# Kernel optimization log

Measured on AMD Instinct MI355X. Metric: run time of the kernel, lower is better.

Reference implementation:

```python
import jax, jax.numpy as jnp
import numpy as np

B, C, H, W = 1, 96, 512, 512
WS, HEADS, SHIFT = 8, 6, 4  # index=1 -> shift = ws//2


def _rel_pos_index(ws):
    # static numpy computation of Swin relative position index, (N, N) int
    coords = np.stack(np.meshgrid(np.arange(ws), np.arange(ws), indexing='ij'))
    cf = coords.reshape(2, -1)                    # (2, N)
    rel = (cf[:, :, None] - cf[:, None, :]).transpose(1, 2, 0)  # (N, N, 2)
    rel[:, :, 0] += ws - 1
    rel[:, :, 1] += ws - 1
    rel[:, :, 0] *= 2 * ws - 1
    return rel.sum(-1)                            # (N, N)


def _attn_mask(h, w, ws, shift):
    # static numpy replication of calculate_mask (shift>0 assumed meaningful)
    img = np.zeros((h, w), np.float32)
    sl = (slice(0, -ws), slice(-ws, -shift), slice(-shift, None))
    cnt = 0
    for hs in sl:
        for wcol in sl:
            img[hs, wcol] = cnt
            cnt += 1
    mw = img.reshape(h // ws, ws, w // ws, ws).transpose(0, 2, 1, 3).reshape(-1, ws * ws)
    am = mw[:, None, :] - mw[:, :, None]          # (nW, N, N)
    return np.where(am != 0, np.float32(-100.0), np.float32(0.0))


def setup_inputs() -> dict:
    key = jax.random.key(0)
    ks = jax.random.split(key, 5)
    return {
        "x": jax.random.normal(ks[0], (B, C, H, W), jnp.float32),
        "rel_bias_table": jax.random.normal(ks[1], ((2 * WS - 1) ** 2, HEADS), jnp.float32) * 0.02,
        "w_qkv": jax.random.normal(ks[2], (3 * C, C), jnp.float32) * 0.02,
        "b_qkv": jnp.zeros((3 * C,), jnp.float32),
        "w_proj": jax.random.normal(ks[3], (C, C), jnp.float32) * 0.02,
        "b_proj": jnp.zeros((C,), jnp.float32),
        "window_size": WS,
        "num_heads": HEADS,
        "shift_size": SHIFT,
    }


def reference(x, rel_bias_table, w_qkv, b_qkv, w_proj, b_proj, window_size, num_heads, shift_size):
    b, c, h, w = x.shape
    ws = window_size
    n = ws * ws
    hd = c // num_heads
    scale = hd ** -0.5

    # faithful to original: raw reshape (B,C,H,W)->(B,H,W,C), roll, reshape back
    xv = x.reshape(b, h, w, c)
    if shift_size > 0:
        xv = jnp.roll(xv, (-shift_size, -shift_size), axis=(1, 2))
    xv = xv.reshape(b, c, h, w)

    # window_partition -> (B_, N, C)
    win = xv.reshape(b, c, h // ws, ws, w // ws, ws).transpose(0, 2, 4, 3, 5, 1).reshape(-1, n, c)
    b_ = win.shape[0]

    qkv = (win @ w_qkv.T + b_qkv).reshape(b_, n, 3, num_heads, hd).transpose(2, 0, 3, 1, 4)
    q, k, v = qkv[0] * scale, qkv[1], qkv[2]       # (B_, h, N, hd)

    attn = jnp.einsum('bhnd,bhmd->bhnm', q, k)     # (B_, h, N, N)

    idx = _rel_pos_index(ws)
    bias = rel_bias_table[idx.reshape(-1)].reshape(n, n, num_heads).transpose(2, 0, 1)
    attn = attn + bias[None]

    mask = jnp.asarray(_attn_mask(h, w, ws, shift_size))  # (nW, N, N)
    nw = mask.shape[0]
    attn = (attn.reshape(b_ // nw, nw, num_heads, n, n) + mask[None, :, None]).reshape(b_, num_heads, n, n)

    attn = jax.nn.softmax(attn, axis=-1)
    out = jnp.einsum('bhnm,bhmd->bhnd', attn, v).transpose(0, 2, 1, 3).reshape(b_, n, c)
    out = out @ w_proj.T + b_proj

    # window_reverse -> (B, C, H, W)
    return out.reshape(b, h // ws, w // ws, ws, ws, c).transpose(0, 5, 1, 3, 2, 4).reshape(b, c, h, w)
```

## Files before the change

### kernel.cpp

```cpp
#include <hip/hip_runtime.h>


namespace {
constexpr int kH = 512, kW = 512, kC = 96;
constexpr int kWS = 8, kN = 64, kNH = 6;
constexpr int kShift = 4;
constexpr int kHW = kH * kW;
constexpr int kWC = kW * kC;

constexpr int XT_STRIDE = 97;
constexpr int XT_OFF = 0;
constexpr int QKV_STRIDE = 20;
constexpr int Q_OFF = XT_OFF + kN * XT_STRIDE;
constexpr int K_OFF = Q_OFF + kN * QKV_STRIDE;
constexpr int V_OFF = K_OFF + kN * QKV_STRIDE;
constexpr int BIAS_OFF = V_OFF + kN * QKV_STRIDE;
constexpr int LAB_OFF = BIAS_OFF + 225 * kNH;
constexpr int POOL = LAB_OFF + kN;
}

__global__ __launch_bounds__(256, 3) void swin_window_attn(
    const float* __restrict__ x,
    const float* __restrict__ bias_tab,
    const float* __restrict__ w_qkv,
    const float* __restrict__ b_qkv,
    const float* __restrict__ w_proj,
    const float* __restrict__ b_proj,
    float* __restrict__ out) {
  __shared__ __align__(16) float pool[POOL];
  float* xt = pool + XT_OFF;
  float* qS = pool + Q_OFF;
  float* kS = pool + K_OFF;
  float* vS = pool + V_OFF;
  float* biasS = pool + BIAS_OFF;
  int* labS = (int*)(pool + LAB_OFF);

  const int t = threadIdx.x;
  const int lane = t & 63;
  const int wv = __builtin_amdgcn_readfirstlane(t >> 6);
  const int win = blockIdx.x;
  const int wh = win >> 6;
  const int wwi = win & 63;
  const int h0 = wh * kWS;
  const int w0 = wwi * kWS;

  for (int e = t; e < kN * kC; e += 256) {
    const int n = e & 63;
    const int c = e >> 6;
    const int hh = h0 + (n >> 3);
    const int ww = w0 + (n & 7);
    const int idx = c * kHW + hh * kW + ww;
    const int hp = idx / kWC;
    const int rem = idx - hp * kWC;
    const int wp = rem / kC;
    const int cp = rem - wp * kC;
    int hs = hp + kShift; if (hs >= kH) hs -= kH;
    int wsr = wp + kShift; if (wsr >= kW) wsr -= kW;
    xt[n * XT_STRIDE + c] = x[hs * kWC + wsr * kC + cp];
  }
  for (int e = t; e < 225 * kNH; e += 256) {
    const int hb = e / 225;
    const int i = e - hb * 225;
    biasS[e] = bias_tab[i * kNH + hb];
  }
  if (t < kN) {
    const int hh = h0 + (t >> 3);
    const int ww = w0 + (t & 7);
    const int lh = (hh < kH - kWS) ? 0 : (hh < kH - kShift ? 1 : 2);
    const int lw = (ww < kW - kWS) ? 0 : (ww < kW - kShift ? 1 : 2);
    labS[t] = lh * 3 + lw;
  }
  __syncthreads();

  const int cg = lane & 3;
  const int gl = lane & ~3;
  const int r = (wv << 4) + (lane >> 2);
  const int i1 = r >> 3, j1 = r & 7;

  float4 y0 = make_float4(0,0,0,0), y1 = y0, y2 = y0,
         y3 = y0, y4 = y0, y5 = y0;

#pragma unroll 1
  for (int h = 0; h < kNH; ++h) {
    const int row_q = h * 16 + (wv << 2);
    const float* __restrict__ wqp = w_qkv + row_q * kC;
    const float* __restrict__ wkp = w_qkv + (96 + row_q) * kC;
    const float* __restrict__ wvp = w_qkv + (192 + row_q) * kC;
    float aq[4], ak[4], av[4];
#pragma unroll
    for (int u = 0; u < 4; ++u) {
      aq[u] = b_qkv[row_q + u];
      ak[u] = b_qkv[96 + row_q + u];
      av[u] = b_qkv[192 + row_q + u];
    }
    const float* xrow = xt + lane * XT_STRIDE;
    for (int c = 0; c < kC; c += 4) {
      const float xv0 = xrow[c + 0];
      const float xv1 = xrow[c + 1];
      const float xv2 = xrow[c + 2];
      const float xv3 = xrow[c + 3];
#pragma unroll
      for (int u = 0; u < 4; ++u) {
        const float4 wq = *(const float4*)(wqp + u * kC + c);
        aq[u] += xv0 * wq.x + xv1 * wq.y + xv2 * wq.z + xv3 * wq.w;
        const float4 wk = *(const float4*)(wkp + u * kC + c);
        ak[u] += xv0 * wk.x + xv1 * wk.y + xv2 * wk.z + xv3 * wk.w;
        const float4 wvv = *(const float4*)(wvp + u * kC + c);
        av[u] += xv0 * wvv.x + xv1 * wvv.y + xv2 * wvv.z + xv3 * wvv.w;
      }
    }
    *(float4*)(qS + lane * QKV_STRIDE + (wv << 2)) =
        make_float4(aq[0] * 0.25f, aq[1] * 0.25f, aq[2] * 0.25f, aq[3] * 0.25f);
    *(float4*)(kS + lane * QKV_STRIDE + (wv << 2)) =
        make_float4(ak[0], ak[1], ak[2], ak[3]);
    *(float4*)(vS + lane * QKV_STRIDE + (wv << 2)) =
        make_float4(av[0], av[1], av[2], av[3]);
    __syncthreads();

    const float4 qv0 = *(const float4*)(qS + r * QKV_STRIDE + 0);
    const float4 qv1 = *(const float4*)(qS + r * QKV_STRIDE + 4);
    const float4 qv2 = *(const float4*)(qS + r * QKV_STRIDE + 8);
    const float4 qv3 = *(const float4*)(qS + r * QKV_STRIDE + 12);
    const int labn = labS[r];
    const float* biasH = biasS + h * 225;
    float sreg[16];
    float mx = -1e30f;
#pragma unroll
    for (int m = 0; m < 16; ++m) {
      const int col = (cg << 4) + m;
      const float4 k0 = *(const float4*)(kS + col * QKV_STRIDE + 0);
      const float4 k1 = *(const float4*)(kS + col * QKV_STRIDE + 4);
      const float4 k2 = *(const float4*)(kS + col * QKV_STRIDE + 8);
      const float4 k3 = *(const float4*)(kS + col * QKV_STRIDE + 12);
      float s = qv0.x * k0.x + qv0.y * k0.y + qv0.z * k0.z + qv0.w * k0.w
              + qv1.x * k1.x + qv1.y * k1.y + qv1.z * k1.z + qv1.w * k1.w
              + qv2.x * k2.x + qv2.y * k2.y + qv2.z * k2.z + qv2.w * k2.w
              + qv3.x * k3.x + qv3.y * k3.y + qv3.z * k3.z + qv3.w * k3.w;
      s += biasH[(i1 - (col >> 3) + 7) * 15 + (j1 - (col & 7) + 7)];
      s += (labS[col] != labn) ? -100.0f : 0.0f;
      sreg[m] = s;
      mx = fmaxf(mx, s);
    }
    mx = fmaxf(mx, __shfl_xor(mx, 1));
    mx = fmaxf(mx, __shfl_xor(mx, 2));
    float sum = 0.f;
#pragma unroll
    for (int m = 0; m < 16; ++m) {
      const float e = __expf(sreg[m] - mx);
      sreg[m] = e;
      sum += e;
    }
    sum += __shfl_xor(sum, 1);
    sum += __shfl_xor(sum, 2);

    float a0 = 0.f, a1 = 0.f, a2 = 0.f, a3 = 0.f;
#pragma unroll
    for (int s2 = 0; s2 < 16; ++s2) {
#pragma unroll
      for (int g2 = 0; g2 < 4; ++g2) {
        const float p = __shfl(sreg[s2], gl + g2);
        const float4 vvv =
            *(const float4*)(vS + ((g2 << 4) + s2) * QKV_STRIDE + (cg << 2));
        a0 += p * vvv.x; a1 += p * vvv.y; a2 += p * vvv.z; a3 += p * vvv.w;
      }
    }
    const float inv = 1.0f / sum;
    const float4 yh = make_float4(a0 * inv, a1 * inv, a2 * inv, a3 * inv);
    if      (h == 0) y0 = yh;
    else if (h == 1) y1 = yh;
    else if (h == 2) y2 = yh;
    else if (h == 3) y3 = yh;
    else if (h == 4) y4 = yh;
    else             y5 = yh;
    __syncthreads();
  }

  {
    float* yw = xt + r * XT_STRIDE + (cg << 2);
    yw[0]  = y0.x; yw[1]  = y0.y; yw[2]  = y0.z; yw[3]  = y0.w;
    yw[16] = y1.x; yw[17] = y1.y; yw[18] = y1.z; yw[19] = y1.w;
    yw[32] = y2.x; yw[33] = y2.y; yw[34] = y2.z; yw[35] = y2.w;
    yw[48] = y3.x; yw[49] = y3.y; yw[50] = y3.z; yw[51] = y3.w;
    yw[64] = y4.x; yw[65] = y4.y; yw[66] = y4.z; yw[67] = y4.w;
    yw[80] = y5.x; yw[81] = y5.y; yw[82] = y5.z; yw[83] = y5.w;
  }
  __syncthreads();

  const int oc0 = wv * 24;
  const int hh = h0 + (lane >> 3);
  const int ww = w0 + (lane & 7);
  const float* yrow = xt + lane * XT_STRIDE;
  float acc[24];
#pragma unroll
  for (int j = 0; j < 24; ++j) acc[j] = b_proj[oc0 + j];
  for (int c = 0; c < kC; c += 2) {
    const float yv0 = yrow[c];
    const float yv1 = yrow[c + 1];
#pragma unroll
    for (int j = 0; j < 24; ++j) {
      const float2 wp2 = *(const float2*)(w_proj + (oc0 + j) * kC + c);
      acc[j] += yv0 * wp2.x + yv1 * wp2.y;
    }
  }
#pragma unroll
  for (int j = 0; j < 24; ++j)
    out[(oc0 + j) * kHW + hh * kW + ww] = acc[j];
}

extern "C" void kernel_launch(void* const* d_in, const int* in_sizes, int n_in,
                              void* d_out, int out_size, void* d_ws, size_t ws_size,
                              hipStream_t stream) {
  const float* x  = (const float*)d_in[0];
  const float* bt = (const float*)d_in[1];
  const float* wq = (const float*)d_in[2];
  const float* bq = (const float*)d_in[3];
  const float* wp = (const float*)d_in[4];
  const float* bp = (const float*)d_in[5];
  float* out = (float*)d_out;
  swin_window_attn<<<dim3(64 * 64), dim3(256), 0, stream>>>(x, bt, wq, bq, wp, bp, out);
}
```

Measured before the change: 927.5 us.

## Drop LDS bias/label tables, use register mask bits and ds_swizzle broadcast

```diff
diff --git a/kernel.cpp b/kernel.cpp
--- a/kernel.cpp
+++ b/kernel.cpp
@@ -14,12 +14,10 @@
 constexpr int Q_OFF = XT_OFF + kN * XT_STRIDE;
 constexpr int K_OFF = Q_OFF + kN * QKV_STRIDE;
 constexpr int V_OFF = K_OFF + kN * QKV_STRIDE;
-constexpr int BIAS_OFF = V_OFF + kN * QKV_STRIDE;
-constexpr int LAB_OFF = BIAS_OFF + 225 * kNH;
-constexpr int POOL = LAB_OFF + kN;
+constexpr int POOL = V_OFF + kN * QKV_STRIDE;
 }
 
-__global__ __launch_bounds__(256, 3) void swin_window_attn(
+__global__ __launch_bounds__(256, 4) void swin_window_attn(
     const float* __restrict__ x,
     const float* __restrict__ bias_tab,
     const float* __restrict__ w_qkv,
@@ -32,8 +30,6 @@
   float* qS = pool + Q_OFF;
   float* kS = pool + K_OFF;
   float* vS = pool + V_OFF;
-  float* biasS = pool + BIAS_OFF;
-  int* labS = (int*)(pool + LAB_OFF);
 
   const int t = threadIdx.x;
   const int lane = t & 63;
@@ -58,30 +54,35 @@
     int wsr = wp + kShift; if (wsr >= kW) wsr -= kW;
     xt[n * XT_STRIDE + c] = x[hs * kWC + wsr * kC + cp];
   }
-  for (int e = t; e < 225 * kNH; e += 256) {
-    const int hb = e / 225;
-    const int i = e - hb * 225;
-    biasS[e] = bias_tab[i * kNH + hb];
-  }
-  if (t < kN) {
-    const int hh = h0 + (t >> 3);
-    const int ww = w0 + (t & 7);
-    const int lh = (hh < kH - kWS) ? 0 : (hh < kH - kShift ? 1 : 2);
-    const int lw = (ww < kW - kWS) ? 0 : (ww < kW - kShift ? 1 : 2);
-    labS[t] = lh * 3 + lw;
-  }
-  __syncthreads();
 
   const int cg = lane & 3;
-  const int gl = lane & ~3;
   const int r = (wv << 4) + (lane >> 2);
   const int i1 = r >> 3, j1 = r & 7;
 
-  float4 y0 = make_float4(0,0,0,0), y1 = y0, y2 = y0,
+  unsigned mlo = 0, mhi = 0;
+  if (wh == 63 || wwi == 63) {
+    const int rh = h0 + (r >> 3), rw = w0 + (r & 7);
+    const int labr = ((rh >= kH - kWS) + (rh >= kH - kShift)) * 3 +
+                     (rw >= kW - kWS) + (rw >= kW - kShift);
+    for (int m2 = 0; m2 < 64; ++m2) {
+      const int ch = h0 + (m2 >> 3), cw2 = w0 + (m2 & 7);
+      const int labc = ((ch >= kH - kWS) + (ch >= kH - kShift)) * 3 +
+                       (cw2 >= kW - kWS) + (cw2 >= kW - kShift);
+      const unsigned bit = (labc != labr) ? 1u : 0u;
+      if (m2 < 32) mlo |= bit << m2; else mhi |= bit << (m2 - 32);
+    }
+  }
+  const unsigned umlo = mlo >> cg, umhi = mhi >> cg;
+
+  __syncthreads();
+
+  float4 y0 = make_float4(0, 0, 0, 0), y1 = y0, y2 = y0,
          y3 = y0, y4 = y0, y5 = y0;
 
 #pragma unroll 1
   for (int h = 0; h < kNH; ++h) {
+    if (h) __syncthreads();
+
     const int row_q = h * 16 + (wv << 2);
     const float* __restrict__ wqp = w_qkv + row_q * kC;
     const float* __restrict__ wkp = w_qkv + (96 + row_q) * kC;
@@ -117,17 +118,23 @@
         make_float4(av[0], av[1], av[2], av[3]);
     __syncthreads();
 
+    float bv[16];
+#pragma unroll
+    for (int m = 0; m < 16; ++m) {
+      const int col = (m << 2) | cg;
+      const int bidx = (i1 - (col >> 3) + 7) * 15 + (j1 - (col & 7) + 7);
+      bv[m] = bias_tab[bidx * kNH + h];
+    }
+
     const float4 qv0 = *(const float4*)(qS + r * QKV_STRIDE + 0);
     const float4 qv1 = *(const float4*)(qS + r * QKV_STRIDE + 4);
     const float4 qv2 = *(const float4*)(qS + r * QKV_STRIDE + 8);
     const float4 qv3 = *(const float4*)(qS + r * QKV_STRIDE + 12);
-    const int labn = labS[r];
-    const float* biasH = biasS + h * 225;
     float sreg[16];
     float mx = -1e30f;
 #pragma unroll
     for (int m = 0; m < 16; ++m) {
-      const int col = (cg << 4) + m;
+      const int col = (m << 2) | cg;
       const float4 k0 = *(const float4*)(kS + col * QKV_STRIDE + 0);
       const float4 k1 = *(const float4*)(kS + col * QKV_STRIDE + 4);
       const float4 k2 = *(const float4*)(kS + col * QKV_STRIDE + 8);
@@ -136,8 +143,9 @@
               + qv1.x * k1.x + qv1.y * k1.y + qv1.z * k1.z + qv1.w * k1.w
               + qv2.x * k2.x + qv2.y * k2.y + qv2.z * k2.z + qv2.w * k2.w
               + qv3.x * k3.x + qv3.y * k3.y + qv3.z * k3.z + qv3.w * k3.w;
-      s += biasH[(i1 - (col >> 3) + 7) * 15 + (j1 - (col & 7) + 7)];
-      s += (labS[col] != labn) ? -100.0f : 0.0f;
+      s += bv[m];
+      const unsigned um = (m < 8) ? umlo : umhi;
+      s += ((um >> ((m & 7) << 2)) & 1u) ? -100.0f : 0.0f;
       sreg[m] = s;
       mx = fmaxf(mx, s);
     }
@@ -156,12 +164,18 @@
     float a0 = 0.f, a1 = 0.f, a2 = 0.f, a3 = 0.f;
 #pragma unroll
     for (int s2 = 0; s2 < 16; ++s2) {
+      const int pbits = __float_as_int(sreg[s2]);
+      float pb[4];
+      pb[0] = __int_as_float(__builtin_amdgcn_ds_swizzle(pbits, 0x001C));
+      pb[1] = __int_as_float(__builtin_amdgcn_ds_swizzle(pbits, 0x003C));
+      pb[2] = __int_as_float(__builtin_amdgcn_ds_swizzle(pbits, 0x005C));
+      pb[3] = __int_as_float(__builtin_amdgcn_ds_swizzle(pbits, 0x007C));
 #pragma unroll
       for (int g2 = 0; g2 < 4; ++g2) {
-        const float p = __shfl(sreg[s2], gl + g2);
         const float4 vvv =
-            *(const float4*)(vS + ((g2 << 4) + s2) * QKV_STRIDE + (cg << 2));
-        a0 += p * vvv.x; a1 += p * vvv.y; a2 += p * vvv.z; a3 += p * vvv.w;
+            *(const float4*)(vS + ((s2 << 2) | g2) * QKV_STRIDE + (cg << 2));
+        a0 += pb[g2] * vvv.x; a1 += pb[g2] * vvv.y;
+        a2 += pb[g2] * vvv.z; a3 += pb[g2] * vvv.w;
       }
     }
     const float inv = 1.0f / sum;
@@ -172,7 +186,6 @@
     else if (h == 3) y3 = yh;
     else if (h == 4) y4 = yh;
     else             y5 = yh;
-    __syncthreads();
   }
 
   {
```

New measurement: 923.1 us. About the same (-0.5%).
